# Performance work log

Measured on AMD Instinct MI355X. Metric: run time of the kernel, lower is better.

## Reference

```python
import jax, jax.numpy as jnp
import numpy as np

B, P, M, CI, CO, W = 8, 16384, 16, 16, 32, 17
RES_RATE = 0.5
SQ_CONV = float(np.sqrt(1.0 - RES_RATE))
SQ_RES = float(np.sqrt(RES_RATE))


def setup_inputs() -> dict:
    key = jax.random.key(0)
    k0, k1, k2, k3, k4 = jax.random.split(key, 5)
    in_pc = jax.random.normal(k0, (B, P, CI), dtype=jnp.float32)
    # neighbor ids in [0, P]; value P is the padding sentinel (masked out)
    neighbor_id = jax.random.randint(k1, (P, M), 0, P + 1)
    weights = jax.random.normal(k2, (W, CO * CI), dtype=jnp.float32)
    bias = jnp.zeros((P, CO), dtype=jnp.float32)  # perpoint_bias == 1
    w_weights = jax.random.normal(k3, (P, M, W), dtype=jnp.float32) / (M * W)
    weight_res = jax.random.normal(k4, (CO, CI), dtype=jnp.float32) / CO
    return {
        "in_pc": in_pc,
        "weights": weights,
        "bias": bias,
        "w_weights": w_weights,
        "weight_res": weight_res,
        "neighbor_id": neighbor_id,
    }


def reference(in_pc, weights, bias, w_weights, weight_res, neighbor_id):
    b = in_pc.shape[0]
    # mask: 1 for real neighbor, 0 for padding sentinel (id == P)
    mask = (neighbor_id != P).astype(in_pc.dtype)  # [P, M]
    # pad point cloud with one zero point so sentinel index gathers zeros
    in_pc_pad = jnp.concatenate(
        [in_pc, jnp.zeros((b, 1, CI), dtype=in_pc.dtype)], axis=1
    )  # [B, P+1, CI]
    in_neighbors = in_pc_pad[:, neighbor_id]  # [B, P, M, CI]
    # per-point conv weights: masked learned combination of basis weights
    ww = w_weights * mask[:, :, None]  # [P, M, W]
    Wpm = jnp.einsum("pmw,wc->pmc", ww, weights).reshape(P, M, CO, CI)
    # gather-generate-matmul: contract neighbors with per-point weights, sum over M
    out_pc_conv = jnp.einsum("pmoi,bpmi->bpo", Wpm, in_neighbors) + bias
    out_pc_conv = jax.nn.elu(out_pc_conv)  # not final layer
    # residual branch: channel projection (in_c != out_c), identity over points
    out_pc_res = jnp.einsum("oi,bpi->bpo", weight_res, in_pc_pad)[:, :P]
    return out_pc_conv * SQ_CONV + out_pc_res * SQ_RES
```

## Files before the change

### kernel.cpp

```cpp
#include <hip/hip_runtime.h>

#define PP 16384
#define SQH 0.70710678118654752440f

typedef unsigned int u32;
typedef unsigned short u16;
typedef __attribute__((ext_vector_type(8))) short bfrag;
typedef __attribute__((ext_vector_type(4))) float ffrag;
typedef __attribute__((ext_vector_type(16))) float ffrag16;
typedef __attribute__((ext_vector_type(4))) float f4;

union BU { bfrag v; uint4 u; };

__device__ __forceinline__ u32 pk2(float a, float b) {
  u32 ua = __float_as_uint(a), ub = __float_as_uint(b);
  return ((ua + 0x8000u) >> 16) | ((ub + 0x8000u) & 0xffff0000u);
}

#define XTB_B ((size_t)(PP + 1) * 256)
#define WB_B  XTB_B
#define WR_B  (XTB_B + 18432)

__global__ __launch_bounds__(256) void prep_kernel(
    const float* __restrict__ in_pc, const float* __restrict__ weights,
    const float* __restrict__ weight_res, u32* __restrict__ ws) {
  __shared__ u32 T[64 * 72];
  const int blk = blockIdx.x, t = threadIdx.x;
  if (blk < 256) {
    const int p0 = blk * 64;
    const int pl = t >> 2, i4 = t & 3;
#pragma unroll
    for (int b = 0; b < 8; ++b) {
      f4 v = *(const f4*)(in_pc + ((size_t)b * PP + p0 + pl) * 16 + i4 * 4);
      T[pl * 72 + b * 8 + i4 * 2]     = pk2(v.x, v.y);
      T[pl * 72 + b * 8 + i4 * 2 + 1] = pk2(v.z, v.w);
    }
    __syncthreads();
#pragma unroll
    for (int k = 0; k < 4; ++k) {
      int idx = k * 256 + t;
      int pl2 = idx >> 4, c2 = (idx & 15) * 4;
      uint4 v = *(const uint4*)&T[pl2 * 72 + c2];
      *(uint4*)&ws[(size_t)(p0 + pl2) * 64 + c2] = v;
    }
    return;
  }
  if (blk == 256 && t < 32)
    *(uint2*)&ws[(size_t)PP * 64 + t * 2] = make_uint2(0u, 0u);
  int e = (blk - 256) * 256 + t;
  if (e < 1152) {
    int nt = e / 576, rem = e - nt * 576;
    int ks = rem >> 6, l = rem & 63;
    int quad = l >> 4, n = l & 15;
    int k0 = ks * 32 + quad * 8;
    uint4 pkd = make_uint4(0u, 0u, 0u, 0u);
    if (k0 < 272) {
      int w = k0 >> 4, i0 = k0 & 15;
      const float* src = weights + w * 512 + (nt * 16 + n) * 16 + i0;
      f4 lo = *(const f4*)src;
      f4 hi = *(const f4*)(src + 4);
      pkd = make_uint4(pk2(lo.x, lo.y), pk2(lo.z, lo.w), pk2(hi.x, hi.y), pk2(hi.z, hi.w));
    }
    *(uint4*)((char*)ws + WB_B + (size_t)e * 16) = pkd;
  } else if (e < 1280) {
    int l2 = e - 1152, nt = l2 >> 6, l = l2 & 63;
    int quad = l >> 4, n = l & 15;
    uint4 pkd = make_uint4(0u, 0u, 0u, 0u);
    if (quad < 2) {
      const float* src = weight_res + (nt * 16 + n) * 16 + quad * 8;
      f4 lo = *(const f4*)src;
      f4 hi = *(const f4*)(src + 4);
      pkd = make_uint4(pk2(lo.x, lo.y), pk2(lo.z, lo.w), pk2(hi.x, hi.y), pk2(hi.z, hi.w));
    }
    *(uint4*)((char*)ws + WR_B + (size_t)(e - 1152) * 16) = pkd;
  }
}

__global__ __launch_bounds__(256, 4) void pconv_main(
    const u32* __restrict__ ws,
    const float* __restrict__ bias,
    const float* __restrict__ wwg,
    const int*  __restrict__ nidg,
    float* __restrict__ out)
{
  __shared__ __attribute__((aligned(16))) u16 Abuf[4 * 16 * 296];

  const u16*  __restrict__ xTb = (const u16*)ws;
  const uint4* __restrict__ WB = (const uint4*)((const char*)ws + WB_B);
  const uint4* __restrict__ WR = (const uint4*)((const char*)ws + WR_B);

  const int tid = threadIdx.x;
  const int wid = __builtin_amdgcn_readfirstlane(tid >> 6);
  const int lane = tid & 63;
  const int lo16 = lane & 15, quad = lane >> 4;
  const int col = lane & 31, h = lane >> 5;
  u16* __restrict__ Aw = Abuf + wid * (16 * 296);

  const int p0 = (blockIdx.x * 4 + wid) * 2;

  {
    int r = lane >> 2, c = lane & 3;
    *(uint2*)(Aw + r * 296 + 272 + c * 4) = make_uint2(0u, 0u);
  }

  int nid0[16], nid1[16];
#pragma unroll
  for (int m = 0; m < 16; ++m) nid0[m] = nidg[(size_t)p0 * 16 + m];
#pragma unroll
  for (int m = 0; m < 16; ++m) nid1[m] = nidg[(size_t)(p0 + 1) * 16 + m];

  BU bb0, bb1;
  {
    float v0[8], v1[8];
#pragma unroll
    for (int idx = 0; idx < 8; ++idx) {
      float x0 = 0.f, x1 = 0.f;
      if (col < 17) {
        x0 = wwg[(size_t)p0 * 272 + (h * 8 + idx) * 17 + col];
        x1 = wwg[(size_t)(p0 + 1) * 272 + (h * 8 + idx) * 17 + col];
      }
      v0[idx] = x0; v1[idx] = x1;
    }
    bb0.u = make_uint4(pk2(v0[0], v0[1]), pk2(v0[2], v0[3]), pk2(v0[4], v0[5]), pk2(v0[6], v0[7]));
    bb1.u = make_uint4(pk2(v1[0], v1[1]), pk2(v1[2], v1[3]), pk2(v1[4], v1[5]), pk2(v1[6], v1[7]));
  }

  const int voffb = (col >> 4) * 16 + (col & 15);
  u32 a0[4][4], a1[4][4];
#pragma unroll
  for (int j = 0; j < 4; ++j) {
    const u16* q0 = xTb + (size_t)nid0[h * 8 + 2 * j] * 128 + voffb;
    const u16* q1 = xTb + (size_t)nid0[h * 8 + 2 * j + 1] * 128 + voffb;
#pragma unroll
    for (int t = 0; t < 4; ++t)
      a0[t][j] = (u32)q0[t * 32] | ((u32)q1[t * 32] << 16);
  }
#pragma unroll
  for (int j = 0; j < 4; ++j) {
    const u16* q0 = xTb + (size_t)nid1[h * 8 + 2 * j] * 128 + voffb;
    const u16* q1 = xTb + (size_t)nid1[h * 8 + 2 * j + 1] * 128 + voffb;
#pragma unroll
    for (int t = 0; t < 4; ++t)
      a1[t][j] = (u32)q0[t * 32] | ((u32)q1[t * 32] << 16);
  }

  float blo[4], bhi[4];
#pragma unroll
  for (int j = 0; j < 4; ++j) {
    int p_e = p0 + ((quad * 4 + j) >> 3);
    blo[j] = bias[(size_t)p_e * 32 + lo16];
    bhi[j] = bias[(size_t)p_e * 32 + 16 + lo16];
  }
  BU su;
  su.u = make_uint4(0u, 0u, 0u, 0u);
  {
    const int p_r = p0 + (lo16 >> 3), b_r = lo16 & 7;
    if (quad < 2)
      su.u = *(const uint4*)(xTb + (size_t)p_r * 128 + b_r * 16 + quad * 8);
  }
  BU rb0, rb1;
  rb0.u = WR[lane];
  rb1.u = WR[64 + lane];

#pragma unroll
  for (int pt = 0; pt < 2; ++pt) {
    const u32 (&ad)[4][4] = pt ? a1 : a0;
    BU bb = pt ? bb1 : bb0;
#pragma unroll
    for (int t = 0; t < 4; ++t) {
      BU aa;
      aa.u = make_uint4(ad[t][0], ad[t][1], ad[t][2], ad[t][3]);
      ffrag16 c = {};
      c = __builtin_amdgcn_mfma_f32_32x32x16_bf16(aa.v, bb.v, c, 0, 0, 0);
      if (col < 17) {
#pragma unroll
        for (int q = 0; q < 4; ++q) {
          int r = pt * 8 + 2 * t + (q >> 1);
          int i0 = 4 * h + 8 * (q & 1);
          u16* dst = Aw + r * 296 + col * 16 + i0;
          *(uint2*)dst = make_uint2(pk2(c[4 * q + 0], c[4 * q + 1]),
                                    pk2(c[4 * q + 2], c[4 * q + 3]));
        }
      }
    }
  }

  ffrag acc0 = {0.f, 0.f, 0.f, 0.f}, acc1 = {0.f, 0.f, 0.f, 0.f};
#pragma unroll
  for (int ks = 0; ks < 9; ++ks) {
    bfrag af = *(const bfrag*)(Aw + lo16 * 296 + ks * 32 + quad * 8);
    BU b0, b1;
    b0.u = WB[ks * 64 + lane];
    b1.u = WB[576 + ks * 64 + lane];
    acc0 = __builtin_amdgcn_mfma_f32_16x16x32_bf16(af, b0.v, acc0, 0, 0, 0);
    acc1 = __builtin_amdgcn_mfma_f32_16x16x32_bf16(af, b1.v, acc1, 0, 0, 0);
  }
  ffrag rz = {0.f, 0.f, 0.f, 0.f};
  ffrag res0 = __builtin_amdgcn_mfma_f32_16x16x32_bf16(su.v, rb0.v, rz, 0, 0, 0);
  ffrag res1 = __builtin_amdgcn_mfma_f32_16x16x32_bf16(su.v, rb1.v, rz, 0, 0, 0);

  float* Ef = (float*)Aw;
#pragma unroll
  for (int j = 0; j < 4; ++j) {
    int r = quad * 4 + j;
    float c0 = acc0[j] + blo[j];
    float c1 = acc1[j] + bhi[j];
    float e0 = c0 > 0.f ? c0 : (__expf(c0) - 1.f);
    float e1 = c1 > 0.f ? c1 : (__expf(c1) - 1.f);
    Ef[r * 40 + lo16]      = SQH * e0 + SQH * res0[j];
    Ef[r * 40 + 16 + lo16] = SQH * e1 + SQH * res1[j];
  }
#pragma unroll
  for (int k = 0; k < 2; ++k) {
    int rr = (lane >> 3) + 8 * k;
    int cc = lane & 7;
    f4 v = *(const f4*)(Ef + rr * 40 + cc * 4);
    int p_s = p0 + (rr >> 3), b_s = rr & 7;
    *(f4*)(out + ((size_t)b_s * PP + p_s) * 32 + cc * 4) = v;
  }
}

extern "C" void kernel_launch(void* const* d_in, const int* in_sizes, int n_in,
                              void* d_out, int out_size, void* d_ws, size_t ws_size,
                              hipStream_t stream) {
  const float* in_pc       = (const float*)d_in[0];
  const float* weights     = (const float*)d_in[1];
  const float* bias        = (const float*)d_in[2];
  const float* w_weights   = (const float*)d_in[3];
  const float* weight_res  = (const float*)d_in[4];
  const int*   neighbor_id = (const int*)d_in[5];
  float* out = (float*)d_out;
  u32* ws = (u32*)d_ws;

  hipLaunchKernelGGL(prep_kernel, dim3(261), dim3(256), 0, stream,
                     in_pc, weights, weight_res, ws);
  hipLaunchKernelGGL(pconv_main, dim3(2048), dim3(256), 0, stream,
                     ws, bias, w_weights, neighbor_id, out);
}
```

Baseline: 102.6 us.

## Process four points per wave with software-prefetched neighbor gathers

Each wave now handles two pairs of points instead of one, and the grid is halved. The gathers for the second pair are issued right after the first pair's weight-generation MFMAs, so their latency overlaps the first pair's weight-basis MFMAs and epilogue. This adds register pressure (nid for four points, more fragments) and halves the number of blocks, which may reduce occupancy and latency hiding across waves.

```diff
diff --git a/kernel.cpp b/kernel.cpp
--- a/kernel.cpp
+++ b/kernel.cpp
@@ -76,6 +76,19 @@
   }
 }
 
+__device__ __forceinline__ void gather_pt(u32 (&ad)[4][4], const int (&nd)[16],
+                                          const u16* __restrict__ xTb,
+                                          int h, int voffb) {
+#pragma unroll
+  for (int j = 0; j < 4; ++j) {
+    const u16* q0 = xTb + (size_t)nd[h * 8 + 2 * j] * 128 + voffb;
+    const u16* q1 = xTb + (size_t)nd[h * 8 + 2 * j + 1] * 128 + voffb;
+#pragma unroll
+    for (int t = 0; t < 4; ++t)
+      ad[t][j] = (u32)q0[t * 32] | ((u32)q1[t * 32] << 16);
+  }
+}
+
 __global__ __launch_bounds__(256, 4) void pconv_main(
     const u32* __restrict__ ws,
     const float* __restrict__ bias,
@@ -96,127 +109,130 @@
   const int col = lane & 31, h = lane >> 5;
   u16* __restrict__ Aw = Abuf + wid * (16 * 296);
 
-  const int p0 = (blockIdx.x * 4 + wid) * 2;
+  const int pbase = (blockIdx.x * 4 + wid) * 4;
 
   {
     int r = lane >> 2, c = lane & 3;
     *(uint2*)(Aw + r * 296 + 272 + c * 4) = make_uint2(0u, 0u);
   }
 
-  int nid0[16], nid1[16];
-#pragma unroll
-  for (int m = 0; m < 16; ++m) nid0[m] = nidg[(size_t)p0 * 16 + m];
-#pragma unroll
-  for (int m = 0; m < 16; ++m) nid1[m] = nidg[(size_t)(p0 + 1) * 16 + m];
-
-  BU bb0, bb1;
-  {
-    float v0[8], v1[8];
+  int nid[4][16];
+#pragma unroll
+  for (int p = 0; p < 4; ++p)
+#pragma unroll
+    for (int m = 0; m < 16; ++m)
+      nid[p][m] = nidg[(size_t)(pbase + p) * 16 + m];
+
+  BU bb[4];
+#pragma unroll
+  for (int p = 0; p < 4; ++p) {
+    float v[8];
 #pragma unroll
     for (int idx = 0; idx < 8; ++idx) {
-      float x0 = 0.f, x1 = 0.f;
-      if (col < 17) {
-        x0 = wwg[(size_t)p0 * 272 + (h * 8 + idx) * 17 + col];
-        x1 = wwg[(size_t)(p0 + 1) * 272 + (h * 8 + idx) * 17 + col];
-      }
-      v0[idx] = x0; v1[idx] = x1;
-    }
-    bb0.u = make_uint4(pk2(v0[0], v0[1]), pk2(v0[2], v0[3]), pk2(v0[4], v0[5]), pk2(v0[6], v0[7]));
-    bb1.u = make_uint4(pk2(v1[0], v1[1]), pk2(v1[2], v1[3]), pk2(v1[4], v1[5]), pk2(v1[6], v1[7]));
-  }
-
-  const int voffb = (col >> 4) * 16 + (col & 15);
-  u32 a0[4][4], a1[4][4];
-#pragma unroll
-  for (int j = 0; j < 4; ++j) {
-    const u16* q0 = xTb + (size_t)nid0[h * 8 + 2 * j] * 128 + voffb;
-    const u16* q1 = xTb + (size_t)nid0[h * 8 + 2 * j + 1] * 128 + voffb;
-#pragma unroll
-    for (int t = 0; t < 4; ++t)
-      a0[t][j] = (u32)q0[t * 32] | ((u32)q1[t * 32] << 16);
-  }
-#pragma unroll
-  for (int j = 0; j < 4; ++j) {
-    const u16* q0 = xTb + (size_t)nid1[h * 8 + 2 * j] * 128 + voffb;
-    const u16* q1 = xTb + (size_t)nid1[h * 8 + 2 * j + 1] * 128 + voffb;
-#pragma unroll
-    for (int t = 0; t < 4; ++t)
-      a1[t][j] = (u32)q0[t * 32] | ((u32)q1[t * 32] << 16);
-  }
-
-  float blo[4], bhi[4];
-#pragma unroll
-  for (int j = 0; j < 4; ++j) {
-    int p_e = p0 + ((quad * 4 + j) >> 3);
-    blo[j] = bias[(size_t)p_e * 32 + lo16];
-    bhi[j] = bias[(size_t)p_e * 32 + 16 + lo16];
-  }
-  BU su;
-  su.u = make_uint4(0u, 0u, 0u, 0u);
-  {
-    const int p_r = p0 + (lo16 >> 3), b_r = lo16 & 7;
-    if (quad < 2)
-      su.u = *(const uint4*)(xTb + (size_t)p_r * 128 + b_r * 16 + quad * 8);
-  }
+      float x = 0.f;
+      if (col < 17)
+        x = wwg[(size_t)(pbase + p) * 272 + (h * 8 + idx) * 17 + col];
+      v[idx] = x;
+    }
+    bb[p].u = make_uint4(pk2(v[0], v[1]), pk2(v[2], v[3]),
+                         pk2(v[4], v[5]), pk2(v[6], v[7]));
+  }
+
   BU rb0, rb1;
   rb0.u = WR[lane];
   rb1.u = WR[64 + lane];
-
-#pragma unroll
-  for (int pt = 0; pt < 2; ++pt) {
-    const u32 (&ad)[4][4] = pt ? a1 : a0;
-    BU bb = pt ? bb1 : bb0;
-#pragma unroll
-    for (int t = 0; t < 4; ++t) {
-      BU aa;
-      aa.u = make_uint4(ad[t][0], ad[t][1], ad[t][2], ad[t][3]);
-      ffrag16 c = {};
-      c = __builtin_amdgcn_mfma_f32_32x32x16_bf16(aa.v, bb.v, c, 0, 0, 0);
-      if (col < 17) {
-#pragma unroll
-        for (int q = 0; q < 4; ++q) {
-          int r = pt * 8 + 2 * t + (q >> 1);
-          int i0 = 4 * h + 8 * (q & 1);
-          u16* dst = Aw + r * 296 + col * 16 + i0;
-          *(uint2*)dst = make_uint2(pk2(c[4 * q + 0], c[4 * q + 1]),
-                                    pk2(c[4 * q + 2], c[4 * q + 3]));
+  BU su[2];
+#pragma unroll
+  for (int pp = 0; pp < 2; ++pp) {
+    su[pp].u = make_uint4(0u, 0u, 0u, 0u);
+    const int p_r = pbase + 2 * pp + (lo16 >> 3), b_r = lo16 & 7;
+    if (quad < 2)
+      su[pp].u = *(const uint4*)(xTb + (size_t)p_r * 128 + b_r * 16 + quad * 8);
+  }
+
+  const int voffb = (col >> 4) * 16 + (col & 15);
+  u32 a0[4][4], a1[4][4];
+  gather_pt(a0, nid[0], xTb, h, voffb);
+  gather_pt(a1, nid[1], xTb, h, voffb);
+
+#pragma unroll
+  for (int pp = 0; pp < 2; ++pp) {
+    const int p0 = pbase + 2 * pp;
+
+#pragma unroll
+    for (int pt = 0; pt < 2; ++pt) {
+      const u32 (&ad)[4][4] = pt ? a1 : a0;
+      BU bbv = bb[2 * pp + pt];
+#pragma unroll
+      for (int t = 0; t < 4; ++t) {
+        BU aa;
+        aa.u = make_uint4(ad[t][0], ad[t][1], ad[t][2], ad[t][3]);
+        ffrag16 c = {};
+        c = __builtin_amdgcn_mfma_f32_32x32x16_bf16(aa.v, bbv.v, c, 0, 0, 0);
+        if (col < 17) {
+#pragma unroll
+          for (int q = 0; q < 4; ++q) {
+            int r = pt * 8 + 2 * t + (q >> 1);
+            int i0 = 4 * h + 8 * (q & 1);
+            u16* dst = Aw + r * 296 + col * 16 + i0;
+            *(uint2*)dst = make_uint2(pk2(c[4 * q + 0], c[4 * q + 1]),
+                                      pk2(c[4 * q + 2], c[4 * q + 3]));
+          }
         }
       }
     }
-  }
-
-  ffrag acc0 = {0.f, 0.f, 0.f, 0.f}, acc1 = {0.f, 0.f, 0.f, 0.f};
-#pragma unroll
-  for (int ks = 0; ks < 9; ++ks) {
-    bfrag af = *(const bfrag*)(Aw + lo16 * 296 + ks * 32 + quad * 8);
-    BU b0, b1;
-    b0.u = WB[ks * 64 + lane];
-    b1.u = WB[576 + ks * 64 + lane];
-    acc0 = __builtin_amdgcn_mfma_f32_16x16x32_bf16(af, b0.v, acc0, 0, 0, 0);
-    acc1 = __builtin_amdgcn_mfma_f32_16x16x32_bf16(af, b1.v, acc1, 0, 0, 0);
-  }
-  ffrag rz = {0.f, 0.f, 0.f, 0.f};
-  ffrag res0 = __builtin_amdgcn_mfma_f32_16x16x32_bf16(su.v, rb0.v, rz, 0, 0, 0);
-  ffrag res1 = __builtin_amdgcn_mfma_f32_16x16x32_bf16(su.v, rb1.v, rz, 0, 0, 0);
-
-  float* Ef = (float*)Aw;
-#pragma unroll
-  for (int j = 0; j < 4; ++j) {
-    int r = quad * 4 + j;
-    float c0 = acc0[j] + blo[j];
-    float c1 = acc1[j] + bhi[j];
-    float e0 = c0 > 0.f ? c0 : (__expf(c0) - 1.f);
-    float e1 = c1 > 0.f ? c1 : (__expf(c1) - 1.f);
-    Ef[r * 40 + lo16]      = SQH * e0 + SQH * res0[j];
-    Ef[r * 40 + 16 + lo16] = SQH * e1 + SQH * res1[j];
-  }
-#pragma unroll
-  for (int k = 0; k < 2; ++k) {
-    int rr = (lane >> 3) + 8 * k;
-    int cc = lane & 7;
-    f4 v = *(const f4*)(Ef + rr * 40 + cc * 4);
-    int p_s = p0 + (rr >> 3), b_s = rr & 7;
-    *(f4*)(out + ((size_t)b_s * PP + p_s) * 32 + cc * 4) = v;
+
+    if (pp == 0) {
+      gather_pt(a0, nid[2], xTb, h, voffb);
+      gather_pt(a1, nid[3], xTb, h, voffb);
+    }
+
+    float blo[4], bhi[4];
+#pragma unroll
+    for (int j = 0; j < 4; ++j) {
+      int p_e = p0 + ((quad * 4 + j) >> 3);
+      blo[j] = bias[(size_t)p_e * 32 + lo16];
+      bhi[j] = bias[(size_t)p_e * 32 + 16 + lo16];
+    }
+
+    ffrag acc0 = {0.f, 0.f, 0.f, 0.f}, acc1 = {0.f, 0.f, 0.f, 0.f};
+#pragma unroll
+    for (int ks = 0; ks < 9; ++ks) {
+      bfrag af = *(const bfrag*)(Aw + lo16 * 296 + ks * 32 + quad * 8);
+      BU b0, b1;
+      b0.u = WB[ks * 64 + lane];
+      b1.u = WB[576 + ks * 64 + lane];
+      acc0 = __builtin_amdgcn_mfma_f32_16x16x32_bf16(af, b0.v, acc0, 0, 0, 0);
+      acc1 = __builtin_amdgcn_mfma_f32_16x16x32_bf16(af, b1.v, acc1, 0, 0, 0);
+    }
+    ffrag rz = {0.f, 0.f, 0.f, 0.f};
+    ffrag res0 = __builtin_amdgcn_mfma_f32_16x16x32_bf16(su[pp].v, rb0.v, rz, 0, 0, 0);
+    ffrag res1 = __builtin_amdgcn_mfma_f32_16x16x32_bf16(su[pp].v, rb1.v, rz, 0, 0, 0);
+
+    float* Ef = (float*)Aw;
+#pragma unroll
+    for (int j = 0; j < 4; ++j) {
+      int r = quad * 4 + j;
+      float c0 = acc0[j] + blo[j];
+      float c1 = acc1[j] + bhi[j];
+      float e0 = c0 > 0.f ? c0 : (__expf(c0) - 1.f);
+      float e1 = c1 > 0.f ? c1 : (__expf(c1) - 1.f);
+      Ef[r * 40 + lo16]      = SQH * e0 + SQH * res0[j];
+      Ef[r * 40 + 16 + lo16] = SQH * e1 + SQH * res1[j];
+    }
+#pragma unroll
+    for (int k = 0; k < 2; ++k) {
+      int rr = (lane >> 3) + 8 * k;
+      int cc = lane & 7;
+      f4 v = *(const f4*)(Ef + rr * 40 + cc * 4);
+      int p_s = p0 + (rr >> 3), b_s = rr & 7;
+      *(f4*)(out + ((size_t)b_s * PP + p_s) * 32 + cc * 4) = v;
+    }
+
+    if (pp == 0) {
+      int r = lane >> 2, c = lane & 3;
+      *(uint2*)(Aw + r * 296 + 272 + c * 4) = make_uint2(0u, 0u);
+    }
   }
 }
 
@@ -234,6 +250,6 @@
 
   hipLaunchKernelGGL(prep_kernel, dim3(261), dim3(256), 0, stream,
                      in_pc, weights, weight_res, ws);
-  hipLaunchKernelGGL(pconv_main, dim3(2048), dim3(256), 0, stream,
+  hipLaunchKernelGGL(pconv_main, dim3(1024), dim3(256), 0, stream,
                      ws, bias, w_weights, neighbor_id, out);
 }
```

After: 139.4 us. 35.9% more time.
